# Optimization experiments

Hardware: AMD Instinct MI355X
Metric: run time of the kernel (lower is better)

The kernel has to match this reference:

```python
import jax, jax.numpy as jnp
import numpy as np

N = 20000      # nodes
E = 160000     # edges (avg degree 16)
IN_DIM = 256
HID = 128      # hidden_dim == per-head out_channels in PyG TransformerConv
HEADS = 4
EPS = 1e-5


def setup_inputs() -> dict:
    key = jax.random.key(0)
    ks = jax.random.split(key, 24)

    def w(k, shape, scale=0.05):
        return jax.random.normal(k, shape, dtype=jnp.float32) * scale

    inp = {
        "x": jax.random.normal(ks[0], (N, IN_DIM), dtype=jnp.float32),
        "edge_index": jax.random.randint(ks[1], (2, E), 0, N, dtype=jnp.int32),
        # input projection
        "lin_w": w(ks[2], (IN_DIM, HID)), "lin_b": jnp.zeros((HID,), jnp.float32),
    }
    i = 3
    for l in (1, 2):
        inp[f"q_w{l}"] = w(ks[i], (HID, HEADS * HID)); i += 1
        inp[f"q_b{l}"] = jnp.zeros((HEADS * HID,), jnp.float32)
        inp[f"k_w{l}"] = w(ks[i], (HID, HEADS * HID)); i += 1
        inp[f"k_b{l}"] = jnp.zeros((HEADS * HID,), jnp.float32)
        inp[f"v_w{l}"] = w(ks[i], (HID, HEADS * HID)); i += 1
        inp[f"v_b{l}"] = jnp.zeros((HEADS * HID,), jnp.float32)
        inp[f"s_w{l}"] = w(ks[i], (HID, HID)); i += 1
        inp[f"s_b{l}"] = jnp.zeros((HID,), jnp.float32)
        inp[f"ln_g{l}"] = jnp.ones((HID,), jnp.float32)
        inp[f"ln_b{l}"] = jnp.zeros((HID,), jnp.float32)
    return inp


def _segment_softmax(scores, seg, num):
    # scores: [E, HEADS], seg: [E] destination indices
    m = jax.ops.segment_max(scores, seg, num_segments=num)
    m = jnp.where(jnp.isfinite(m), m, 0.0)  # guard empty segments
    e = jnp.exp(scores - m[seg])
    d = jax.ops.segment_sum(e, seg, num_segments=num)
    return e / (d[seg] + 1e-16)


def _transformer_conv(x, src, dst, qw, qb, kw, kb, vw, vb, sw, sb):
    # PyG TransformerConv(HID, HID, heads=HEADS, concat=False)
    n = x.shape[0]
    q = (x @ qw + qb).reshape(n, HEADS, HID)
    k = (x @ kw + kb).reshape(n, HEADS, HID)
    v = (x @ vw + vb).reshape(n, HEADS, HID)
    # per-edge attention: query at dst (i), key/value at src (j)
    alpha = jnp.einsum("ehd,ehd->eh", q[dst], k[src]) / jnp.sqrt(jnp.float32(HID))
    alpha = _segment_softmax(alpha, dst, n)                 # [E, HEADS]
    msg = v[src] * alpha[..., None]                          # [E, HEADS, HID]
    out = jax.ops.segment_sum(msg, dst, num_segments=n)      # [N, HEADS, HID]
    out = out.mean(axis=1)                                   # concat=False -> head mean
    return out + x @ sw + sb                                 # root skip connection


def _layer_norm(x, g, b):
    mu = x.mean(-1, keepdims=True)
    var = ((x - mu) ** 2).mean(-1, keepdims=True)
    return (x - mu) * jax.lax.rsqrt(var + EPS) * g + b


def reference(x, edge_index, lin_w, lin_b,
              q_w1, q_b1, k_w1, k_b1, v_w1, v_b1, s_w1, s_b1, ln_g1, ln_b1,
              q_w2, q_b2, k_w2, k_b2, v_w2, v_b2, s_w2, s_b2, ln_g2, ln_b2):
    src, dst = edge_index[0], edge_index[1]
    h = jax.nn.relu(x @ lin_w + lin_b)
    h1 = _transformer_conv(h, src, dst, q_w1, q_b1, k_w1, k_b1, v_w1, v_b1, s_w1, s_b1)
    h = _layer_norm(h1 + h, ln_g1, ln_b1)
    h2 = _transformer_conv(h, src, dst, q_w2, q_b2, k_w2, k_b2, v_w2, v_b2, s_w2, s_b2)
    h = _layer_norm(h2 + h, ln_g2, ln_b2)
    return h
```

## Files before the change

### kernel.cpp

```cpp
#include <hip/hip_runtime.h>
#include <math.h>

#define NNODE 20000
#define NEDGE 160000
#define IN_DIMV 256
#define HIDV 128
#define DEGCAP 64
#define BAT 4

typedef __attribute__((ext_vector_type(8))) short bf16x8;
typedef __attribute__((ext_vector_type(4))) float f32x4;
typedef __attribute__((ext_vector_type(2))) float f32x2;

__device__ __forceinline__ float bf2f(unsigned short u) {
    union { unsigned int i; float f; } x; x.i = ((unsigned int)u) << 16; return x.f;
}
__device__ __forceinline__ unsigned short f2bf(float f) {
    union { float f; unsigned int i; } x; x.f = f;
    unsigned int r = x.i + 0x7fffu + ((x.i >> 16) & 1u);
    return (unsigned short)(r >> 16);
}
__device__ __forceinline__ void unpack8(uint4 p, float* f) {
    f[0] = bf2f((unsigned short)(p.x & 0xffff)); f[1] = bf2f((unsigned short)(p.x >> 16));
    f[2] = bf2f((unsigned short)(p.y & 0xffff)); f[3] = bf2f((unsigned short)(p.y >> 16));
    f[4] = bf2f((unsigned short)(p.z & 0xffff)); f[5] = bf2f((unsigned short)(p.z >> 16));
    f[6] = bf2f((unsigned short)(p.w & 0xffff)); f[7] = bf2f((unsigned short)(p.w >> 16));
}
__device__ __forceinline__ void unpack8f8_w(unsigned int a, unsigned int b, float* f) {
    f32x2 t;
    t = __builtin_amdgcn_cvt_pk_f32_fp8((int)a, false); f[0] = t.x; f[1] = t.y;
    t = __builtin_amdgcn_cvt_pk_f32_fp8((int)a, true);  f[2] = t.x; f[3] = t.y;
    t = __builtin_amdgcn_cvt_pk_f32_fp8((int)b, false); f[4] = t.x; f[5] = t.y;
    t = __builtin_amdgcn_cvt_pk_f32_fp8((int)b, true);  f[6] = t.x; f[7] = t.y;
}
__device__ __forceinline__ unsigned char f2fp8(float v) {
    int pk = __builtin_amdgcn_cvt_pk_fp8_f32(v, v, 0, false);
    return (unsigned char)(pk & 0xff);
}
__device__ __forceinline__ void gld_lds16(const unsigned short* g, unsigned short* l) {
    __builtin_amdgcn_global_load_lds((const __attribute__((address_space(1))) void*)g,
                                     (__attribute__((address_space(3))) void*)l, 16, 0, 0);
}
__device__ __forceinline__ void gld_lds16b(const unsigned char* g, unsigned char* l) {
    __builtin_amdgcn_global_load_lds((const __attribute__((address_space(1))) void*)g,
                                     (__attribute__((address_space(3))) void*)l, 16, 0, 0);
}

__global__ void convert_kernel(
    const float* __restrict__ lin_w,
    const float* __restrict__ qw0, const float* __restrict__ kw0,
    const float* __restrict__ vw0, const float* __restrict__ sw0,
    const float* __restrict__ qw1, const float* __restrict__ kw1,
    const float* __restrict__ vw1, const float* __restrict__ sw1,
    unsigned short* __restrict__ arena, int* __restrict__ cursor)
{
    int idx = blockIdx.x * 256 + threadIdx.x;
    if (idx < NNODE) cursor[idx] = 0;
    int id2 = idx - NNODE;
    if (id2 < 0 || id2 >= 458752) return;
    float v;
    if (id2 < 32768) {
        int n = id2 >> 8, k = id2 & 255;
        v = lin_w[k * 128 + n];
    } else {
        int t = id2 - 32768;
        int l = t / 212992, r = t % 212992;
        int n = r >> 7, k = r & 127;
        const float* qw = l ? qw1 : qw0;
        const float* kw = l ? kw1 : kw0;
        const float* vw = l ? vw1 : vw0;
        const float* sw = l ? sw1 : sw0;
        if (n < 1536) {
            const float* w = (n < 512) ? qw : (n < 1024) ? kw : vw;
            v = w[k * 512 + (n & 511)];
        } else {
            v = sw[k * 128 + (n - 1536)];
        }
    }
    arena[id2] = f2bf(v);
}

__global__ __launch_bounds__(256) void mfma_gemm0(
    const float* __restrict__ A, const unsigned short* __restrict__ WT,
    const float* __restrict__ b0, unsigned short* __restrict__ hbf_out)
{
    __shared__ unsigned short smem[8192];
    unsigned short* As = smem;
    unsigned short* Bs = smem + 4096;
    unsigned short* ot = smem;
    const int K = 256;

    int tid = threadIdx.x;
    int lane = tid & 63;
    int w = tid >> 6;
    int wm = w & 1, wn = w >> 1;
    int bm = blockIdx.x * 128;

    int r0 = tid >> 2;
    int c0 = (tid & 3) * 8;
    int g0 = bm + r0;      if (g0 > NNODE - 1) g0 = NNODE - 1;
    int g1 = bm + r0 + 64; if (g1 > NNODE - 1) g1 = NNODE - 1;
    int srow = lane >> 2;
    int scol = (lane & 3) * 8;
    int br0 = w * 32 + srow;
    int br1 = w * 32 + 16 + srow;

    f32x4 acc[4][4] = {};
    int arow = wm * 64 + (lane & 15);
    int brow = wn * 64 + (lane & 15);
    int koff = (lane >> 4) * 8;

    for (int k0 = 0; k0 < K; k0 += 32) {
        {
            const float4* p0 = (const float4*)(A + (size_t)g0 * K + k0 + c0);
            float4 u = p0[0], v = p0[1];
            unsigned short t0[8] = {f2bf(u.x), f2bf(u.y), f2bf(u.z), f2bf(u.w),
                                    f2bf(v.x), f2bf(v.y), f2bf(v.z), f2bf(v.w)};
            *(uint4*)&As[r0 * 32 + c0] = *(uint4*)t0;
            const float4* p1 = (const float4*)(A + (size_t)g1 * K + k0 + c0);
            u = p1[0]; v = p1[1];
            unsigned short t1[8] = {f2bf(u.x), f2bf(u.y), f2bf(u.z), f2bf(u.w),
                                    f2bf(v.x), f2bf(v.y), f2bf(v.z), f2bf(v.w)};
            *(uint4*)&As[(r0 + 64) * 32 + c0] = *(uint4*)t1;
        }
        gld_lds16(WT + (size_t)br0 * K + k0 + scol, Bs + (w * 32) * 32);
        gld_lds16(WT + (size_t)br1 * K + k0 + scol, Bs + (w * 32 + 16) * 32);
        __syncthreads();
        bf16x8 fa[4], fb[4];
#pragma unroll
        for (int i = 0; i < 4; i++) fa[i] = *(const bf16x8*)&As[(arow + i * 16) * 32 + koff];
#pragma unroll
        for (int i = 0; i < 4; i++) fb[i] = *(const bf16x8*)&Bs[(brow + i * 16) * 32 + koff];
#pragma unroll
        for (int mi = 0; mi < 4; mi++)
#pragma unroll
            for (int ni = 0; ni < 4; ni++)
                acc[mi][ni] = __builtin_amdgcn_mfma_f32_16x16x32_bf16(fa[mi], fb[ni], acc[mi][ni], 0, 0, 0);
        __syncthreads();
    }

    int quad = lane >> 4, lcol = lane & 15;
#pragma unroll
    for (int hh = 0; hh < 2; hh++) {
        __syncthreads();
        if (wm == hh) {
#pragma unroll
            for (int mi = 0; mi < 4; mi++) {
#pragma unroll
                for (int ni = 0; ni < 4; ni++) {
                    int lc = wn * 64 + ni * 16 + lcol;
                    float bias = b0[lc];
#pragma unroll
                    for (int reg = 0; reg < 4; reg++) {
                        float v = fmaxf(acc[mi][ni][reg] + bias, 0.f);
                        ot[(mi * 16 + quad * 4 + reg) * 128 + lc] = f2bf(v);
                    }
                }
            }
        }
        __syncthreads();
        int r = tid >> 2, ch = tid & 3;
        int row = bm + hh * 64 + r;
        if (row < NNODE) {
            uint4* dp = (uint4*)(hbf_out + (size_t)row * HIDV + ch * 32);
            const uint4* sp = (const uint4*)(ot + r * 128 + ch * 32);
#pragma unroll
            for (int q = 0; q < 4; q++) dp[q] = sp[q];
        }
    }
}

__global__ __launch_bounds__(256) void mfma_gemm1(
    const unsigned short* __restrict__ A, const unsigned short* __restrict__ WT,
    const float* __restrict__ b0, const float* __restrict__ b1,
    const float* __restrict__ b2, const float* __restrict__ b3,
    unsigned short* __restrict__ qb_out, unsigned char* __restrict__ kv8_out,
    unsigned short* __restrict__ pre16_out)
{
    __shared__ unsigned short As[16384];
    __shared__ unsigned short Ws[16384];
    unsigned short* ot = Ws;
    unsigned char* ot8 = (unsigned char*)Ws;
    const int K = 128;

    int tid = threadIdx.x;
    int lane = tid & 63;
    int w = tid >> 6;
    int wm = w & 1, wn = w >> 1;
    int bm = blockIdx.x * 128;
    int p0 = (blockIdx.y == 0) ? 0 : 7;
    int p1 = (blockIdx.y == 0) ? 7 : 13;

    int srow = lane >> 2;
    int scol = (lane & 3) * 8;
    int sr0 = w * 32 + srow;
    int sr1 = w * 32 + 16 + srow;
    int ar0 = bm + sr0; if (ar0 > NNODE - 1) ar0 = NNODE - 1;
    int ar1 = bm + sr1; if (ar1 > NNODE - 1) ar1 = NNODE - 1;

#pragma unroll
    for (int c = 0; c < 4; c++) {
        int k0 = c * 32;
        gld_lds16(A + (size_t)ar0 * K + k0 + scol, As + c * 4096 + sr0 * 32);
        gld_lds16(A + (size_t)ar1 * K + k0 + scol, As + c * 4096 + sr1 * 32);
    }

    int arow = wm * 64 + (lane & 15);
    int brow = wn * 64 + (lane & 15);
    int koff = (lane >> 4) * 8;
    int quad = lane >> 4, lcol = lane & 15;

    for (int p = p0; p < p1; p++) {
        int bn = p * 128;
#pragma unroll
        for (int c = 0; c < 4; c++) {
            int k0 = c * 32;
            gld_lds16(WT + (size_t)(bn + sr0) * K + k0 + scol, Ws + c * 4096 + sr0 * 32);
            gld_lds16(WT + (size_t)(bn + sr1) * K + k0 + scol, Ws + c * 4096 + sr1 * 32);
        }
        __syncthreads();

        f32x4 acc[4][4] = {};
#pragma unroll
        for (int c = 0; c < 4; c++) {
            bf16x8 fa[4], fb[4];
#pragma unroll
            for (int i = 0; i < 4; i++) fa[i] = *(const bf16x8*)&As[c * 4096 + (arow + i * 16) * 32 + koff];
#pragma unroll
            for (int i = 0; i < 4; i++) fb[i] = *(const bf16x8*)&Ws[c * 4096 + (brow + i * 16) * 32 + koff];
#pragma unroll
            for (int mi = 0; mi < 4; mi++)
#pragma unroll
                for (int ni = 0; ni < 4; ni++)
                    acc[mi][ni] = __builtin_amdgcn_mfma_f32_16x16x32_bf16(fa[mi], fb[ni], acc[mi][ni], 0, 0, 0);
        }
        __syncthreads();

        if (p < 4 || p == 12) {
            const float* bb = (p < 4) ? (b0 + bn) : b3;
#pragma unroll
            for (int mi = 0; mi < 4; mi++) {
#pragma unroll
                for (int ni = 0; ni < 4; ni++) {
                    int lc = wn * 64 + ni * 16 + lcol;
                    float bias = bb[lc];
#pragma unroll
                    for (int reg = 0; reg < 4; reg++)
                        ot[(wm * 64 + mi * 16 + quad * 4 + reg) * 128 + lc] = f2bf(acc[mi][ni][reg] + bias);
                }
            }
            __syncthreads();
            int r = tid >> 1, hf = tid & 1;
            int row = bm + r;
            if (row < NNODE) {
                unsigned short* dst = (p < 4) ? (qb_out + (size_t)row * 512 + bn + hf * 64)
                                              : (pre16_out + (size_t)row * HIDV + hf * 64);
                const uint4* sp = (const uint4*)(ot + r * 128 + hf * 64);
                uint4* dp = (uint4*)dst;
#pragma unroll
                for (int q = 0; q < 8; q++) dp[q] = sp[q];
            }
            __syncthreads();
        } else {
            const float* bb = (bn < 1024) ? (b1 + bn - 512) : (b2 + bn - 1024);
            int coff = bn - 512;
#pragma unroll
            for (int mi = 0; mi < 4; mi++) {
#pragma unroll
                for (int ni = 0; ni < 4; ni++) {
                    int lc = wn * 64 + ni * 16 + lcol;
                    float bias = bb[lc];
#pragma unroll
                    for (int reg = 0; reg < 4; reg++)
                        ot8[(wm * 64 + mi * 16 + quad * 4 + reg) * 128 + lc] = f2fp8(acc[mi][ni][reg] + bias);
                }
            }
            __syncthreads();
            int r = tid >> 1, hf = tid & 1;
            int row = bm + r;
            if (row < NNODE) {
                uint4* dp = (uint4*)(kv8_out + (size_t)row * 1024 + coff + hf * 64);
                const uint4* sp = (const uint4*)(ot8 + r * 128 + hf * 64);
#pragma unroll
                for (int q = 0; q < 4; q++) dp[q] = sp[q];
            }
            __syncthreads();
        }
    }
}

__global__ void scatter_kernel(const int* __restrict__ ei, int* __restrict__ cursor,
                               int* __restrict__ bucket) {
    int e = blockIdx.x * blockDim.x + threadIdx.x;
    if (e < NEDGE) {
        int d = ei[NEDGE + e];
        int slot = atomicAdd(&cursor[d], 1);
        if (slot < DEGCAP) bucket[d * DEGCAP + slot] = ei[e];
    }
}

__global__ __launch_bounds__(256) void attn_ln_kernel(
    const unsigned short* __restrict__ qb, const unsigned char* __restrict__ kv8,
    const int* __restrict__ cursor, const int* __restrict__ bucket,
    const unsigned short* __restrict__ pre16, const float* __restrict__ g,
    const float* __restrict__ b,
    unsigned short* __restrict__ hbf ,
    float* __restrict__ extout)
{
    __shared__ __align__(16) unsigned char ring[4][2][BAT * 1024];
    int lane = threadIdx.x & 63;
    int wid = threadIdx.x >> 6;
    int i = blockIdx.x * 4 + wid;
    int cnt = cursor[i]; if (cnt > DEGCAP) cnt = DEGCAP;
    const int* bk = bucket + i * DEGCAP;

    int hg = lane >> 4;
    int sl = lane & 15;

    float qr[8];
    {
        uint4 p = *(const uint4*)(qb + (size_t)i * 512 + lane * 8);
        unpack8(p, qr);
#pragma unroll
        for (int j = 0; j < 8; j++) qr[j] *= 0.0883883476483184f;
    }

    float m = -INFINITY, l = 0.f;
    float acc[8] = {0.f, 0.f, 0.f, 0.f, 0.f, 0.f, 0.f, 0.f};

    if (cnt > 0) {
        int myidx = bk[(lane < cnt) ? lane : 0];

        auto issue = [&](int bb, unsigned char* half) {
#pragma unroll
            for (int t = 0; t < BAT; t++) {
                int j = bb * BAT + t; if (j >= cnt) j = cnt - 1;
                int src = __shfl(myidx, j);
                gld_lds16b(kv8 + (size_t)src * 1024 + lane * 16, half + t * 1024);
            }
        };

        issue(0, ring[wid][0]);
        for (int bb = 0; bb * BAT < cnt; bb++) {
            unsigned char* cur = ring[wid][bb & 1];
            unsigned char* nxt = ring[wid][(bb + 1) & 1];
            bool more = (bb + 1) * BAT < cnt;
            if (more) {
                asm volatile("s_waitcnt lgkmcnt(0)" ::: "memory");
                issue(bb + 1, nxt);
                asm volatile("s_waitcnt vmcnt(4)" ::: "memory");
            } else {
                asm volatile("s_waitcnt vmcnt(0)" ::: "memory");
            }
            int rem = cnt - bb * BAT;

            float d[BAT];
#pragma unroll
            for (int t = 0; t < BAT; t++) d[t] = -3.0e38f;
#pragma unroll
            for (int t = 0; t < BAT; t++) {
                if (t >= rem) break;
                uint2 kk = *(const uint2*)(cur + t * 1024 + hg * 128 + sl * 8);
                float kf[8];
                unpack8f8_w(kk.x, kk.y, kf);
                d[t] = qr[0] * kf[0] + qr[1] * kf[1] + qr[2] * kf[2] + qr[3] * kf[3] +
                       qr[4] * kf[4] + qr[5] * kf[5] + qr[6] * kf[6] + qr[7] * kf[7];
            }
#pragma unroll
            for (int t = 0; t < BAT; t++) { if (t >= rem) break; d[t] += __shfl_xor(d[t], 8); }
#pragma unroll
            for (int t = 0; t < BAT; t++) { if (t >= rem) break; d[t] += __shfl_xor(d[t], 4); }
#pragma unroll
            for (int t = 0; t < BAT; t++) { if (t >= rem) break; d[t] += __shfl_xor(d[t], 2); }
#pragma unroll
            for (int t = 0; t < BAT; t++) { if (t >= rem) break; d[t] += __shfl_xor(d[t], 1); }

            float mq = d[0];
#pragma unroll
            for (int t = 1; t < BAT; t++) mq = fmaxf(mq, d[t]);
            float mn = fmaxf(m, mq);
            float scale = __expf(m - mn);
            float p[BAT];
            float psum = 0.f;
#pragma unroll
            for (int t = 0; t < BAT; t++) { p[t] = __expf(d[t] - mn); psum += p[t]; }
            l = l * scale + psum;
            m = mn;
#pragma unroll
            for (int c = 0; c < 8; c++) acc[c] *= scale;
#pragma unroll
            for (int t = 0; t < BAT; t++) {
                if (t >= rem) break;
                uint2 vv = *(const uint2*)(cur + t * 1024 + 512 + hg * 128 + sl * 8);
                float vf[8];
                unpack8f8_w(vv.x, vv.y, vf);
                float pt = p[t];
#pragma unroll
                for (int c = 0; c < 8; c++) acc[c] += pt * vf[c];
            }
        }
    }

    float linv = 0.25f / (l + 1e-16f);
#pragma unroll
    for (int c = 0; c < 8; c++) acc[c] *= linv;
#pragma unroll
    for (int c = 0; c < 8; c++) {
        acc[c] += __shfl_xor(acc[c], 16);
        acc[c] += __shfl_xor(acc[c], 32);
    }

    size_t base = (size_t)i * HIDV + sl * 8;
    float pv[8], hv[8];
    unpack8(*(const uint4*)(pre16 + base), pv);
    unpack8(*(const uint4*)(hbf + base), hv);
    float vals[8];
#pragma unroll
    for (int c = 0; c < 8; c++) vals[c] = acc[c] + pv[c] + hv[c];

    float s = 0.f;
#pragma unroll
    for (int c = 0; c < 8; c++) s += vals[c];
    s += __shfl_xor(s, 1); s += __shfl_xor(s, 2);
    s += __shfl_xor(s, 4); s += __shfl_xor(s, 8);
    float mu = s * (1.f / 128.f);
    float vs = 0.f;
#pragma unroll
    for (int c = 0; c < 8; c++) { float dx = vals[c] - mu; vs += dx * dx; }
    vs += __shfl_xor(vs, 1); vs += __shfl_xor(vs, 2);
    vs += __shfl_xor(vs, 4); vs += __shfl_xor(vs, 8);
    float rstd = rsqrtf(vs * (1.f / 128.f) + 1e-5f);

    float4 g0 = ((const float4*)(g + sl * 8))[0];
    float4 g1 = ((const float4*)(g + sl * 8))[1];
    float4 bb0 = ((const float4*)(b + sl * 8))[0];
    float4 bb1 = ((const float4*)(b + sl * 8))[1];
    float y[8];
    y[0] = (vals[0] - mu) * rstd * g0.x + bb0.x; y[1] = (vals[1] - mu) * rstd * g0.y + bb0.y;
    y[2] = (vals[2] - mu) * rstd * g0.z + bb0.z; y[3] = (vals[3] - mu) * rstd * g0.w + bb0.w;
    y[4] = (vals[4] - mu) * rstd * g1.x + bb1.x; y[5] = (vals[5] - mu) * rstd * g1.y + bb1.y;
    y[6] = (vals[6] - mu) * rstd * g1.z + bb1.z; y[7] = (vals[7] - mu) * rstd * g1.w + bb1.w;

    if (lane < 16) {
        unsigned short tmp[8] = {f2bf(y[0]), f2bf(y[1]), f2bf(y[2]), f2bf(y[3]),
                                 f2bf(y[4]), f2bf(y[5]), f2bf(y[6]), f2bf(y[7])};
        *(uint4*)(hbf + base) = *(uint4*)tmp;
        if (extout) {
            ((float4*)(extout + base))[0] = make_float4(y[0], y[1], y[2], y[3]);
            ((float4*)(extout + base))[1] = make_float4(y[4], y[5], y[6], y[7]);
        }
    }
}

extern "C" void kernel_launch(void* const* d_in, const int* in_sizes, int n_in,
                              void* d_out, int out_size, void* d_ws, size_t ws_size,
                              hipStream_t stream) {
    const float* x = (const float*)d_in[0];
    const int* ei = (const int*)d_in[1];

    char* ws = (char*)d_ws;
    unsigned short* hbf = (unsigned short*)(ws + 0);
    unsigned short* pre16 = (unsigned short*)(ws + 5120000);
    unsigned short* qb = (unsigned short*)(ws + 10240000);
    unsigned char* kv8 = (unsigned char*)(ws + 30720000);
    int* cursor = (int*)(ws + 51200000);
    int* bucket = (int*)(ws + 51280000);
    unsigned short* arena = (unsigned short*)(ws + 56400000);

    convert_kernel<<<(NNODE + 458752 + 255) / 256, 256, 0, stream>>>(
        (const float*)d_in[2],
        (const float*)d_in[4], (const float*)d_in[6], (const float*)d_in[8], (const float*)d_in[10],
        (const float*)d_in[14], (const float*)d_in[16], (const float*)d_in[18], (const float*)d_in[20],
        arena, cursor);

    scatter_kernel<<<(NEDGE + 255) / 256, 256, 0, stream>>>(ei, cursor, bucket);

    const int GM = (NNODE + 127) / 128;

    mfma_gemm0<<<GM, 256, 0, stream>>>(x, arena, (const float*)d_in[3], hbf);

    for (int l = 0; l < 2; l++) {
        int o = 4 + l * 10;
        const unsigned short* WT = arena + 32768 + l * 212992;
        mfma_gemm1<<<dim3(GM, 2), 256, 0, stream>>>(
            hbf, WT,
            (const float*)d_in[o + 1], (const float*)d_in[o + 3],
            (const float*)d_in[o + 5], (const float*)d_in[o + 7],
            qb, kv8, pre16);

        attn_ln_kernel<<<NNODE / 4, 256, 0, stream>>>(
            qb, kv8, cursor, bucket, pre16,
            (const float*)d_in[o + 8], (const float*)d_in[o + 9],
            hbf, (l == 1) ? (float*)d_out : nullptr);
    }
}
```

Before: 292.1 us.

## Replace LDS ring buffer with register double-buffered gathers in attention kernel

The attention/LayerNorm kernel stops staging gathered fp8 K/V rows through an LDS ring via global_load_lds. Each lane now loads its 8-byte K and V slices straight into registers, using two register sets (A/B) that alternate between issuing and consuming batches. The residual and pre-activation loads are also moved to the top of the kernel so their latency overlaps the edge loop. This removes the LDS traffic and explicit waitcnt handling and frees shared memory for higher occupancy, at the cost of more VGPRs and smaller 8-byte global loads instead of 16-byte ones.

```diff
diff --git a/kernel.cpp b/kernel.cpp
--- a/kernel.cpp
+++ b/kernel.cpp
@@ -38,10 +38,6 @@
     return (unsigned char)(pk & 0xff);
 }
 __device__ __forceinline__ void gld_lds16(const unsigned short* g, unsigned short* l) {
-    __builtin_amdgcn_global_load_lds((const __attribute__((address_space(1))) void*)g,
-                                     (__attribute__((address_space(3))) void*)l, 16, 0, 0);
-}
-__device__ __forceinline__ void gld_lds16b(const unsigned char* g, unsigned char* l) {
     __builtin_amdgcn_global_load_lds((const __attribute__((address_space(1))) void*)g,
                                      (__attribute__((address_space(3))) void*)l, 16, 0, 0);
 }
@@ -307,7 +303,6 @@
     unsigned short* __restrict__ hbf ,
     float* __restrict__ extout)
 {
-    __shared__ __align__(16) unsigned char ring[4][2][BAT * 1024];
     int lane = threadIdx.x & 63;
     int wid = threadIdx.x >> 6;
     int i = blockIdx.x * 4 + wid;
@@ -316,6 +311,11 @@
 
     int hg = lane >> 4;
     int sl = lane & 15;
+    int off = hg * 128 + sl * 8;
+
+    size_t base = (size_t)i * HIDV + sl * 8;
+    uint4 pv_raw = *(const uint4*)(pre16 + base);
+    uint4 hv_raw = *(const uint4*)(hbf + base);
 
     float qr[8];
     {
@@ -331,38 +331,29 @@
     if (cnt > 0) {
         int myidx = bk[(lane < cnt) ? lane : 0];
 
-        auto issue = [&](int bb, unsigned char* half) {
+        uint2 kA[BAT], vA[BAT], kB[BAT], vB[BAT];
+
+        auto issue = [&](uint2 (&KB)[BAT], uint2 (&VB)[BAT], int bb) {
 #pragma unroll
             for (int t = 0; t < BAT; t++) {
                 int j = bb * BAT + t; if (j >= cnt) j = cnt - 1;
                 int src = __shfl(myidx, j);
-                gld_lds16b(kv8 + (size_t)src * 1024 + lane * 16, half + t * 1024);
+                const unsigned char* bp = kv8 + (size_t)src * 1024 + off;
+                KB[t] = *(const uint2*)bp;
+                VB[t] = *(const uint2*)(bp + 512);
             }
         };
 
-        issue(0, ring[wid][0]);
-        for (int bb = 0; bb * BAT < cnt; bb++) {
-            unsigned char* cur = ring[wid][bb & 1];
-            unsigned char* nxt = ring[wid][(bb + 1) & 1];
-            bool more = (bb + 1) * BAT < cnt;
-            if (more) {
-                asm volatile("s_waitcnt lgkmcnt(0)" ::: "memory");
-                issue(bb + 1, nxt);
-                asm volatile("s_waitcnt vmcnt(4)" ::: "memory");
-            } else {
-                asm volatile("s_waitcnt vmcnt(0)" ::: "memory");
-            }
+        auto consume = [&](const uint2 (&KB)[BAT], const uint2 (&VB)[BAT], int bb) {
             int rem = cnt - bb * BAT;
-
             float d[BAT];
 #pragma unroll
             for (int t = 0; t < BAT; t++) d[t] = -3.0e38f;
 #pragma unroll
             for (int t = 0; t < BAT; t++) {
                 if (t >= rem) break;
-                uint2 kk = *(const uint2*)(cur + t * 1024 + hg * 128 + sl * 8);
                 float kf[8];
-                unpack8f8_w(kk.x, kk.y, kf);
+                unpack8f8_w(KB[t].x, KB[t].y, kf);
                 d[t] = qr[0] * kf[0] + qr[1] * kf[1] + qr[2] * kf[2] + qr[3] * kf[3] +
                        qr[4] * kf[4] + qr[5] * kf[5] + qr[6] * kf[6] + qr[7] * kf[7];
             }
@@ -391,12 +382,22 @@
 #pragma unroll
             for (int t = 0; t < BAT; t++) {
                 if (t >= rem) break;
-                uint2 vv = *(const uint2*)(cur + t * 1024 + 512 + hg * 128 + sl * 8);
                 float vf[8];
-                unpack8f8_w(vv.x, vv.y, vf);
+                unpack8f8_w(VB[t].x, VB[t].y, vf);
                 float pt = p[t];
 #pragma unroll
                 for (int c = 0; c < 8; c++) acc[c] += pt * vf[c];
+            }
+        };
+
+        int nb = (cnt + BAT - 1) >> 2;
+        issue(kA, vA, 0);
+        for (int bb = 0; bb < nb; bb += 2) {
+            if (bb + 1 < nb) issue(kB, vB, bb + 1);
+            consume(kA, vA, bb);
+            if (bb + 1 < nb) {
+                if (bb + 2 < nb) issue(kA, vA, bb + 2);
+                consume(kB, vB, bb + 1);
             }
         }
     }
@@ -410,10 +411,9 @@
         acc[c] += __shfl_xor(acc[c], 32);
     }
 
-    size_t base = (size_t)i * HIDV + sl * 8;
     float pv[8], hv[8];
-    unpack8(*(const uint4*)(pre16 + base), pv);
-    unpack8(*(const uint4*)(hbf + base), hv);
+    unpack8(pv_raw, pv);
+    unpack8(hv_raw, hv);
     float vals[8];
 #pragma unroll
     for (int c = 0; c < 8; c++) vals[c] = acc[c] + pv[c] + hv[c];
```

Measured after the change: 279.5 us. 4.3% less time.
